# Performance work log

Hardware: AMD Instinct MI355X
Metric: run time of the kernel (lower is better)

## Reference

```python
import jax, jax.numpy as jnp
import numpy as np


def setup_inputs() -> dict:
    key = jax.random.key(0)
    k1, k2, k3, k4 = jax.random.split(key, 4)
    B, L, K, E, V = 32, 256, 8, 768, 50000
    hidden_feature = jax.random.normal(k1, (B, L, E), dtype=jnp.float32)
    similar_words_sent = jax.random.randint(k2, (B, L, K), 0, V, dtype=jnp.int64)
    word2vec = jax.random.normal(k3, (V, E), dtype=jnp.float32)
    # xavier_uniform for (E, E)
    limit = float(np.sqrt(6.0 / (E + E)))
    weight = jax.random.uniform(k4, (E, E), dtype=jnp.float32, minval=-limit, maxval=limit)
    return {
        "hidden_feature": hidden_feature,
        "similar_words_sent": similar_words_sent,
        "word2vec": word2vec,
        "weight": weight,
    }


def reference(hidden_feature, similar_words_sent, word2vec, weight):
    # Gather k similar-word embeddings: [B, L, K, E]
    k_sims = word2vec[similar_words_sent]
    # Bilinear attention scores: (q @ W) . k  -> [B, L, K]
    q_proj = jnp.einsum("ble,ef->blf", hidden_feature, weight)
    scores = jnp.einsum("ble,blke->blk", q_proj, k_sims)
    attn = jax.nn.softmax(scores, axis=-1)
    # Dropout is identity in eval / rate 0.
    out = jnp.einsum("blk,blke->ble", attn, k_sims)
    return out
```

## Files before the change

kernel.cpp:

```cpp
#include <hip/hip_runtime.h>
#include <hip/hip_bf16.h>


typedef __attribute__((ext_vector_type(8))) _Float16 f16x8;
typedef __attribute__((ext_vector_type(4))) float f32x4;

__device__ __forceinline__ unsigned short f2h(float f) {
    _Float16 h = (_Float16)f;
    return __builtin_bit_cast(unsigned short, h);
}
__device__ __forceinline__ float h2f(unsigned short u) {
    return (float)__builtin_bit_cast(_Float16, u);
}

__device__ __forceinline__ void gload16(const void* g, void* l) {
    __builtin_amdgcn_global_load_lds(
        (const __attribute__((address_space(1))) unsigned int*)g,
        (__attribute__((address_space(3))) unsigned int*)l, 16, 0, 0);
}

__global__ __launch_bounds__(256) void split_all(const float4* __restrict__ x,
                                                 ushort4* __restrict__ hf, int n4,
                                                 const float* __restrict__ W,
                                                 unsigned short* __restrict__ WfT,
                                                 int K, int N, int ablocks) {
    __shared__ float tile[32][33];
    if ((int)blockIdx.x < ablocks) {
        int i = blockIdx.x * 256 + threadIdx.x;
        const int stride = ablocks * 256;
        for (; i < n4; i += stride) {
            float4 v = x[i];
            ushort4 h;
            h.x = f2h(v.x); h.y = f2h(v.y); h.z = f2h(v.z); h.w = f2h(v.w);
            hf[i] = h;
        }
    } else {
        const int bid = blockIdx.x - ablocks;
        const int nbk = K / 32;
        const int bk = (bid % nbk) * 32, bn = (bid / nbk) * 32;
        const int tx = threadIdx.x & 31, ty = threadIdx.x >> 5;
#pragma unroll
        for (int r = ty; r < 32; r += 8)
            tile[r][tx] = W[(size_t)(bk + r) * N + bn + tx];
        __syncthreads();
#pragma unroll
        for (int r = ty; r < 32; r += 8) {
            float v = tile[tx][r];
            WfT[(size_t)(bn + r) * K + bk + tx] = f2h(v);
        }
    }
}

#define BM 128
#define BN 192
#define BK 64
#define GEMM_K 768
#define GEMM_N 768

__global__ __launch_bounds__(512, 2) void gemm_mfma_f16(
        const unsigned short* __restrict__ Af, const unsigned short* __restrict__ BfT,
        unsigned short* __restrict__ C) {

    const int l   = (blockIdx.x & 7) * 32 + (blockIdx.x >> 3);
    const int bm  = (l >> 2) * BM;
    const int bn  = (l & 3) * BN;

    __shared__ unsigned short lds[2 * 2560 * 8];
    const int BOFF = 1024;
    const int BUF  = 2560;

    const int tid  = threadIdx.x;
    const int lane = tid & 63;
    const int w    = tid >> 6;
    const int lr   = lane & 15, lg = lane >> 4;
    const int wm   = w >> 2, wn = w & 3;

    const int lane8 = lane >> 3;
    const int kcl   = (lane & 7) ^ lane8;

    f32x4 acc[4][3];
#pragma unroll
    for (int m = 0; m < 4; ++m)
#pragma unroll
        for (int n = 0; n < 3; ++n) acc[m][n] = (f32x4){0.f, 0.f, 0.f, 0.f};

    const unsigned short* aB[2];
    const unsigned short* bB[3];
#pragma unroll
    for (int i = 0; i < 2; ++i)
        aB[i] = Af + (size_t)(bm + 16 * w + 8 * i + lane8) * GEMM_K + kcl * 8;
#pragma unroll
    for (int i = 0; i < 3; ++i)
        bB[i] = BfT + (size_t)(bn + 24 * w + 8 * i + lane8) * GEMM_K + kcl * 8;

    auto STAGE = [&](int k0, int buf) {
#pragma unroll
        for (int i = 0; i < 2; ++i)
            gload16(aB[i] + k0, &lds[(size_t)(buf * BUF + 128 * w + 64 * i) * 8]);
#pragma unroll
        for (int i = 0; i < 3; ++i)
            gload16(bB[i] + k0, &lds[(size_t)(buf * BUF + BOFF + 192 * w + 64 * i) * 8]);
    };

    STAGE(0, 0);
    __syncthreads();

#pragma unroll
    for (int it = 0; it < GEMM_K / BK; ++it) {
        const int cur = it & 1;
        if (it + 1 < GEMM_K / BK) STAGE((it + 1) * BK, cur ^ 1);

        const int base = cur * BUF;
#pragma unroll
        for (int ks = 0; ks < 2; ++ks) {
            const int kc = ks * 4 + lg;
            const int kx = kc ^ (lr & 7);
            f16x8 a[4], b[3];
#pragma unroll
            for (int m = 0; m < 4; ++m) {
                int slot = base + (wm * 64 + m * 16 + lr) * 8 + kx;
                a[m] = *(const f16x8*)&lds[(size_t)slot * 8];
            }
#pragma unroll
            for (int n = 0; n < 3; ++n) {
                int slot = base + BOFF + (wn * 48 + n * 16 + lr) * 8 + kx;
                b[n] = *(const f16x8*)&lds[(size_t)slot * 8];
            }
#pragma unroll
            for (int m = 0; m < 4; ++m)
#pragma unroll
                for (int n = 0; n < 3; ++n)
                    acc[m][n] = __builtin_amdgcn_mfma_f32_16x16x32_f16(a[m], b[n], acc[m][n], 0, 0, 0);
        }
        __syncthreads();
    }

#pragma unroll
    for (int m = 0; m < 4; ++m)
#pragma unroll
        for (int n = 0; n < 3; ++n) {
            const int col = bn + wn * 48 + n * 16 + lr;
            const int r0  = bm + wm * 64 + m * 16 + lg * 4;
#pragma unroll
            for (int j = 0; j < 4; ++j)
                C[(size_t)(r0 + j) * GEMM_N + col] = f2h(acc[m][n][j]);
        }
}

__global__ __launch_bounds__(256) void attn_online(
        const unsigned short* __restrict__ qf,
        const int* __restrict__ sws,
        const float* __restrict__ w2v,
        float* __restrict__ out) {
    const int wave = threadIdx.x >> 6;
    const int lane = threadIdx.x & 63;
    const size_t row = (size_t)blockIdx.x * 4 + wave;

    const int4 ia = *(const int4*)(sws + row * 8);
    const int4 ib = *(const int4*)(sws + row * 8 + 4);
    const int id[8] = {ia.x, ia.y, ia.z, ia.w, ib.x, ib.y, ib.z, ib.w};

    const ushort4* q4 = (const ushort4*)(qf + row * 768);
    float4 q[3];
#pragma unroll
    for (int j = 0; j < 3; ++j) {
        ushort4 h = q4[j * 64 + lane];
        q[j].x = h2f(h.x); q[j].y = h2f(h.y); q[j].z = h2f(h.z); q[j].w = h2f(h.w);
    }

    float m = -3.0e38f, l = 0.f;
    float4 o[3];
#pragma unroll
    for (int j = 0; j < 3; ++j) { o[j].x = 0.f; o[j].y = 0.f; o[j].z = 0.f; o[j].w = 0.f; }

#pragma unroll
    for (int k = 0; k < 8; ++k) {
        const float4* kp = (const float4*)(w2v + (size_t)id[k] * 768);
        float4 v[3];
#pragma unroll
        for (int j = 0; j < 3; ++j) v[j] = kp[j * 64 + lane];

        float d = 0.f;
#pragma unroll
        for (int j = 0; j < 3; ++j) {
            d += q[j].x * v[j].x;
            d += q[j].y * v[j].y;
            d += q[j].z * v[j].z;
            d += q[j].w * v[j].w;
        }
#pragma unroll
        for (int s = 1; s < 64; s <<= 1) d += __shfl_xor(d, s);

        const float mn = fmaxf(m, d);
        const float sc = __expf(m - mn);
        const float p  = __expf(d - mn);
        l = l * sc + p;
#pragma unroll
        for (int j = 0; j < 3; ++j) {
            o[j].x = o[j].x * sc + p * v[j].x;
            o[j].y = o[j].y * sc + p * v[j].y;
            o[j].z = o[j].z * sc + p * v[j].z;
            o[j].w = o[j].w * sc + p * v[j].w;
        }
        m = mn;
    }

    const float inv = 1.f / l;
    float4* o4 = (float4*)(out + row * 768);
#pragma unroll
    for (int j = 0; j < 3; ++j) {
        float4 r;
        r.x = o[j].x * inv; r.y = o[j].y * inv; r.z = o[j].z * inv; r.w = o[j].w * inv;
        o4[j * 64 + lane] = r;
    }
}

#define GM_BM 128
#define GM_BN 64
#define GM_BK 16
#define GM_TM 8
#define GM_TN 4

__global__ __launch_bounds__(256) void gemm_qproj(const float* __restrict__ A,
                                                  const float* __restrict__ B,
                                                  float* __restrict__ C,
                                                  int M, int N, int K) {
    __shared__ float As[GM_BK][GM_BM];
    __shared__ float Bs[GM_BK][GM_BN];
    const int tid = threadIdx.x;
    const int tx = tid & 15;
    const int ty = tid >> 4;
    const int bm = blockIdx.x * GM_BM;
    const int bn = blockIdx.y * GM_BN;
    float acc[GM_TM][GM_TN];
#pragma unroll
    for (int i = 0; i < GM_TM; ++i)
#pragma unroll
        for (int j = 0; j < GM_TN; ++j) acc[i][j] = 0.f;
    for (int k0 = 0; k0 < K; k0 += GM_BK) {
#pragma unroll
        for (int i = 0; i < 2; ++i) {
            int idx = tid * 2 + i;
            int row = idx >> 2;
            int c4  = idx & 3;
            float4 v = *(const float4*)(A + (size_t)(bm + row) * K + k0 + c4 * 4);
            As[c4 * 4 + 0][row] = v.x;
            As[c4 * 4 + 1][row] = v.y;
            As[c4 * 4 + 2][row] = v.z;
            As[c4 * 4 + 3][row] = v.w;
        }
        {
            int row = tid >> 4;
            int c4  = tid & 15;
            float4 v = *(const float4*)(B + (size_t)(k0 + row) * N + bn + c4 * 4);
            *(float4*)&Bs[row][c4 * 4] = v;
        }
        __syncthreads();
#pragma unroll
        for (int k = 0; k < GM_BK; ++k) {
            float a[GM_TM], b[GM_TN];
#pragma unroll
            for (int i = 0; i < GM_TM; ++i) a[i] = As[k][ty * GM_TM + i];
#pragma unroll
            for (int j = 0; j < GM_TN; ++j) b[j] = Bs[k][tx * GM_TN + j];
#pragma unroll
            for (int i = 0; i < GM_TM; ++i)
#pragma unroll
                for (int j = 0; j < GM_TN; ++j) acc[i][j] += a[i] * b[j];
        }
        __syncthreads();
    }
#pragma unroll
    for (int i = 0; i < GM_TM; ++i) {
        float4 v;
        v.x = acc[i][0]; v.y = acc[i][1]; v.z = acc[i][2]; v.w = acc[i][3];
        *(float4*)(C + (size_t)(bm + ty * GM_TM + i) * N + bn + tx * GM_TN) = v;
    }
}

__global__ __launch_bounds__(256) void attn_fused(const float* __restrict__ qproj,
                                                  const int* __restrict__ sws,
                                                  const float* __restrict__ w2v,
                                                  float* __restrict__ out) {
    const int wave = threadIdx.x >> 6;
    const int lane = threadIdx.x & 63;
    const size_t row = (size_t)blockIdx.x * 4 + wave;

    const float4* q4 = (const float4*)(qproj + row * 768);
    float4 q[3];
#pragma unroll
    for (int j = 0; j < 3; ++j) q[j] = q4[j * 64 + lane];

    float4 ks[8][3];
    float dot[8];
#pragma unroll
    for (int k = 0; k < 8; ++k) {
        int id = sws[row * 8 + k];
        const float4* kp = (const float4*)(w2v + (size_t)id * 768);
        float d = 0.f;
#pragma unroll
        for (int j = 0; j < 3; ++j) {
            float4 v = kp[j * 64 + lane];
            ks[k][j] = v;
            d += q[j].x * v.x + q[j].y * v.y + q[j].z * v.z + q[j].w * v.w;
        }
        dot[k] = d;
    }
#pragma unroll
    for (int k = 0; k < 8; ++k) {
        float d = dot[k];
#pragma unroll
        for (int m = 1; m < 64; m <<= 1) d += __shfl_xor(d, m);
        dot[k] = d;
    }
    float mx = dot[0];
#pragma unroll
    for (int k = 1; k < 8; ++k) mx = fmaxf(mx, dot[k]);
    float wq[8];
    float s = 0.f;
#pragma unroll
    for (int k = 0; k < 8; ++k) { wq[k] = __expf(dot[k] - mx); s += wq[k]; }
    const float inv = 1.f / s;

    float4 o[3];
#pragma unroll
    for (int j = 0; j < 3; ++j) { o[j].x = 0.f; o[j].y = 0.f; o[j].z = 0.f; o[j].w = 0.f; }
#pragma unroll
    for (int k = 0; k < 8; ++k) {
        const float a = wq[k] * inv;
#pragma unroll
        for (int j = 0; j < 3; ++j) {
            o[j].x += a * ks[k][j].x;
            o[j].y += a * ks[k][j].y;
            o[j].z += a * ks[k][j].z;
            o[j].w += a * ks[k][j].w;
        }
    }
    float4* o4 = (float4*)(out + row * 768);
#pragma unroll
    for (int j = 0; j < 3; ++j) o4[j * 64 + lane] = o[j];
}

extern "C" void kernel_launch(void* const* d_in, const int* in_sizes, int n_in,
                              void* d_out, int out_size, void* d_ws, size_t ws_size,
                              hipStream_t stream) {
    const float* hidden = (const float*)d_in[0];
    const int*   sws    = (const int*)d_in[1];
    const float* w2v    = (const float*)d_in[2];
    const float* weight = (const float*)d_in[3];
    float*       out    = (float*)d_out;

    const int E = 768;
    const int M = in_sizes[0] / E;

    const size_t szA = (size_t)M * E;
    const size_t szB = (size_t)E * E;
    const size_t need = (2 * szA + szB) * sizeof(unsigned short);

    if (ws_size >= need && M == 8192) {
        unsigned short* Af  = (unsigned short*)d_ws;
        unsigned short* WfT = Af + szA;
        unsigned short* Qf  = WfT + szB;

        const int ablocks = 2048;
        const int wblocks = (E / 32) * (E / 32);
        split_all<<<ablocks + wblocks, 256, 0, stream>>>(
            (const float4*)hidden, (ushort4*)Af, M * E / 4,
            weight, WfT, E, E, ablocks);

        dim3 ggrid((M / BM) * (E / BN));
        gemm_mfma_f16<<<ggrid, 512, 0, stream>>>(Af, WfT, Qf);

        attn_online<<<dim3(M / 4), 256, 0, stream>>>(Qf, sws, w2v, out);
    } else {
        float* qproj = out;
        dim3 ggrid(M / GM_BM, E / GM_BN);
        gemm_qproj<<<ggrid, 256, 0, stream>>>(hidden, weight, qproj, M, E, E);
        attn_fused<<<dim3(M / 4), 256, 0, stream>>>(qproj, sws, w2v, out);
    }
}
```

Measured before the change: 61.60 us.

## Fuse fp32-to-fp16 conversion of hidden into GEMM A-tile loading

```diff
diff --git a/kernel.cpp b/kernel.cpp
--- a/kernel.cpp
+++ b/kernel.cpp
@@ -11,6 +11,9 @@
 }
 __device__ __forceinline__ float h2f(unsigned short u) {
     return (float)__builtin_bit_cast(_Float16, u);
+}
+__device__ __forceinline__ unsigned int pk2(float a, float b) {
+    return (unsigned int)f2h(a) | ((unsigned int)f2h(b) << 16);
 }
 
 __device__ __forceinline__ void gload16(const void* g, void* l) {
@@ -19,37 +22,23 @@
         (__attribute__((address_space(3))) unsigned int*)l, 16, 0, 0);
 }
 
-__global__ __launch_bounds__(256) void split_all(const float4* __restrict__ x,
-                                                 ushort4* __restrict__ hf, int n4,
-                                                 const float* __restrict__ W,
-                                                 unsigned short* __restrict__ WfT,
-                                                 int K, int N, int ablocks) {
+__global__ __launch_bounds__(256) void prep_w(const float* __restrict__ W,
+                                              unsigned short* __restrict__ WfT) {
     __shared__ float tile[32][33];
-    if ((int)blockIdx.x < ablocks) {
-        int i = blockIdx.x * 256 + threadIdx.x;
-        const int stride = ablocks * 256;
-        for (; i < n4; i += stride) {
-            float4 v = x[i];
-            ushort4 h;
-            h.x = f2h(v.x); h.y = f2h(v.y); h.z = f2h(v.z); h.w = f2h(v.w);
-            hf[i] = h;
-        }
-    } else {
-        const int bid = blockIdx.x - ablocks;
-        const int nbk = K / 32;
-        const int bk = (bid % nbk) * 32, bn = (bid / nbk) * 32;
-        const int tx = threadIdx.x & 31, ty = threadIdx.x >> 5;
-#pragma unroll
-        for (int r = ty; r < 32; r += 8)
-            tile[r][tx] = W[(size_t)(bk + r) * N + bn + tx];
-        __syncthreads();
-#pragma unroll
-        for (int r = ty; r < 32; r += 8) {
-            float v = tile[tx][r];
-            WfT[(size_t)(bn + r) * K + bk + tx] = f2h(v);
-        }
-    }
-}
+    const int bid = blockIdx.x;
+    const int bk = (bid % 24) * 32, bn = (bid / 24) * 32;
+    const int tx = threadIdx.x & 31, ty = threadIdx.x >> 5;
+#pragma unroll
+    for (int r = ty; r < 32; r += 8)
+        tile[r][tx] = W[(size_t)(bk + r) * 768 + bn + tx];
+    __syncthreads();
+#pragma unroll
+    for (int r = ty; r < 32; r += 8) {
+        float v = tile[tx][r];
+        WfT[(size_t)(bn + r) * 768 + bk + tx] = f2h(v);
+    }
+}
+
 
 #define BM 128
 #define BN 192
@@ -57,8 +46,8 @@
 #define GEMM_K 768
 #define GEMM_N 768
 
-__global__ __launch_bounds__(512, 2) void gemm_mfma_f16(
-        const unsigned short* __restrict__ Af, const unsigned short* __restrict__ BfT,
+__global__ __launch_bounds__(512, 2) void gemm_fusedA(
+        const float* __restrict__ hidden, const unsigned short* __restrict__ BfT,
         unsigned short* __restrict__ C) {
 
     const int l   = (blockIdx.x & 7) * 32 + (blockIdx.x >> 3);
@@ -78,37 +67,56 @@
     const int lane8 = lane >> 3;
     const int kcl   = (lane & 7) ^ lane8;
 
-    f32x4 acc[4][3];
-#pragma unroll
-    for (int m = 0; m < 4; ++m)
-#pragma unroll
-        for (int n = 0; n < 3; ++n) acc[m][n] = (f32x4){0.f, 0.f, 0.f, 0.f};
-
-    const unsigned short* aB[2];
+    const int row0  = tid >> 3,          kcA = tid & 7;
+    const int row1  = (tid + 512) >> 3;
+    const int slot0 = row0 * 8 + (kcA ^ (row0 & 7));
+    const int slot1 = row1 * 8 + (kcA ^ (row1 & 7));
+    const float* aP0 = hidden + (size_t)(bm + row0) * GEMM_K + kcA * 8;
+    const float* aP1 = hidden + (size_t)(bm + row1) * GEMM_K + kcA * 8;
+
     const unsigned short* bB[3];
-#pragma unroll
-    for (int i = 0; i < 2; ++i)
-        aB[i] = Af + (size_t)(bm + 16 * w + 8 * i + lane8) * GEMM_K + kcl * 8;
 #pragma unroll
     for (int i = 0; i < 3; ++i)
         bB[i] = BfT + (size_t)(bn + 24 * w + 8 * i + lane8) * GEMM_K + kcl * 8;
 
-    auto STAGE = [&](int k0, int buf) {
-#pragma unroll
-        for (int i = 0; i < 2; ++i)
-            gload16(aB[i] + k0, &lds[(size_t)(buf * BUF + 128 * w + 64 * i) * 8]);
+    auto BSTAGE = [&](int k0, int buf) {
 #pragma unroll
         for (int i = 0; i < 3; ++i)
             gload16(bB[i] + k0, &lds[(size_t)(buf * BUF + BOFF + 192 * w + 64 * i) * 8]);
     };
 
-    STAGE(0, 0);
+    float4 a0, a1, a2, a3;
+    auto ALOAD = [&](int k0) {
+        a0 = *(const float4*)(aP0 + k0);
+        a1 = *(const float4*)(aP0 + k0 + 4);
+        a2 = *(const float4*)(aP1 + k0);
+        a3 = *(const float4*)(aP1 + k0 + 4);
+    };
+    auto AWRITE = [&](int buf) {
+        uint4 p0 = { pk2(a0.x, a0.y), pk2(a0.z, a0.w), pk2(a1.x, a1.y), pk2(a1.z, a1.w) };
+        uint4 p1 = { pk2(a2.x, a2.y), pk2(a2.z, a2.w), pk2(a3.x, a3.y), pk2(a3.z, a3.w) };
+        *(uint4*)&lds[(size_t)(buf * BUF + slot0) * 8] = p0;
+        *(uint4*)&lds[(size_t)(buf * BUF + slot1) * 8] = p1;
+    };
+
+    f32x4 acc[4][3];
+#pragma unroll
+    for (int m = 0; m < 4; ++m)
+#pragma unroll
+        for (int n = 0; n < 3; ++n) acc[m][n] = (f32x4){0.f, 0.f, 0.f, 0.f};
+
+    BSTAGE(0, 0);
+    ALOAD(0);
+    AWRITE(0);
     __syncthreads();
 
 #pragma unroll
     for (int it = 0; it < GEMM_K / BK; ++it) {
         const int cur = it & 1;
-        if (it + 1 < GEMM_K / BK) STAGE((it + 1) * BK, cur ^ 1);
+        if (it + 1 < GEMM_K / BK) {
+            BSTAGE((it + 1) * BK, cur ^ 1);
+            ALOAD((it + 1) * BK);
+        }
 
         const int base = cur * BUF;
 #pragma unroll
@@ -132,6 +140,7 @@
                 for (int n = 0; n < 3; ++n)
                     acc[m][n] = __builtin_amdgcn_mfma_f32_16x16x32_f16(a[m], b[n], acc[m][n], 0, 0, 0);
         }
+        if (it + 1 < GEMM_K / BK) AWRITE(cur ^ 1);
         __syncthreads();
     }
 
@@ -355,21 +364,16 @@
 
     const size_t szA = (size_t)M * E;
     const size_t szB = (size_t)E * E;
-    const size_t need = (2 * szA + szB) * sizeof(unsigned short);
+    const size_t need = (szA + szB) * sizeof(unsigned short);
 
     if (ws_size >= need && M == 8192) {
-        unsigned short* Af  = (unsigned short*)d_ws;
-        unsigned short* WfT = Af + szA;
+        unsigned short* WfT = (unsigned short*)d_ws;
         unsigned short* Qf  = WfT + szB;
 
-        const int ablocks = 2048;
-        const int wblocks = (E / 32) * (E / 32);
-        split_all<<<ablocks + wblocks, 256, 0, stream>>>(
-            (const float4*)hidden, (ushort4*)Af, M * E / 4,
-            weight, WfT, E, E, ablocks);
+        prep_w<<<576, 256, 0, stream>>>(weight, WfT);
 
         dim3 ggrid((M / BM) * (E / BN));
-        gemm_mfma_f16<<<ggrid, 512, 0, stream>>>(Af, WfT, Qf);
+        gemm_fusedA<<<ggrid, 512, 0, stream>>>(hidden, WfT, Qf);
 
         attn_online<<<dim3(M / 4), 256, 0, stream>>>(Qf, sws, w2v, out);
     } else {
```

After: 61.92 us. No clear change (+0.5%).
